# Kernel tuning notes

Measured on AMD Instinct MI355X. Metric: run time of the kernel, lower is better.

Reference implementation:

```python
import jax, jax.numpy as jnp
import numpy as np

B, S, DM, H, D = 2, 1024, 1024, 16, 64  # batch, seq, d_model, heads, head_dim


def setup_inputs() -> dict:
    key = jax.random.key(0)
    ks = jax.random.split(key, 16)
    sc = 1.0 / np.sqrt(DM)
    scd = 1.0 / np.sqrt(D)
    return {
        "hidden_states": jax.random.normal(ks[0], (B, S, DM), dtype=jnp.float32),
        # frozen base_attn projections
        "Wq": jax.random.normal(ks[1], (DM, DM), dtype=jnp.float32) * sc,
        "bq": jnp.zeros((DM,), dtype=jnp.float32),
        "Wk": jax.random.normal(ks[2], (DM, DM), dtype=jnp.float32) * sc,
        "bk": jnp.zeros((DM,), dtype=jnp.float32),
        "Wv": jax.random.normal(ks[3], (DM, DM), dtype=jnp.float32) * sc,
        "bv": jnp.zeros((DM,), dtype=jnp.float32),
        "Wo": jax.random.normal(ks[4], (DM, DM), dtype=jnp.float32) * sc,
        "bo": jnp.zeros((DM,), dtype=jnp.float32),
        # trainable hedgehog feature maps (per-head Linear(head_dim, head_dim))
        "Wfq": jax.random.normal(ks[5], (D, D), dtype=jnp.float32) * scd,
        "bfq": jnp.zeros((D,), dtype=jnp.float32),
        "Wfk": jax.random.normal(ks[6], (D, D), dtype=jnp.float32) * scd,
        "bfk": jnp.zeros((D,), dtype=jnp.float32),
    }


def _heads(x):
    # (B, S, DM) -> (B, H, S, D)
    return x.reshape(B, S, H, D).transpose(0, 2, 1, 3)


def _feature_map(x, W, b):
    # HedgehogFeatureMap: Linear then concat(exp(x), exp(-x)) along last dim
    y = jnp.einsum('bhsd,ed->bhse', x, W) + b
    return jnp.concatenate([jnp.exp(y), jnp.exp(-y)], axis=-1)  # (B,H,S,2D)


def reference(hidden_states, Wq, bq, Wk, bk, Wv, bv, Wo, bo, Wfq, bfq, Wfk, bfk):
    # base_attn: standard multi-head softmax attention with output_attentions=True
    q = _heads(hidden_states @ Wq.T + bq)
    k = _heads(hidden_states @ Wk.T + bk)
    v = _heads(hidden_states @ Wv.T + bv)
    scores = jnp.einsum('bhmd,bhnd->bhmn', q, k) / jnp.sqrt(jnp.float32(D))
    true_attns = jax.nn.softmax(scores, axis=-1)  # (B,H,S,S)
    ctx = jnp.einsum('bhmn,bhnd->bhmd', true_attns, v)
    outputs = ctx.transpose(0, 2, 1, 3).reshape(B, S, DM) @ Wo.T + bo

    # hedgehog path: feature maps on q/k then sum-normalized quadratic attention
    fq = _feature_map(q, Wfq, bfq)
    fk = _feature_map(k, Wfk, bfk)
    qk = jnp.einsum('bhmd,bhnd->bhmn', fq, fk)
    pred_attns = qk / jnp.sum(qk, axis=-1, keepdims=True)
    return (outputs, pred_attns, true_attns)
```

## Files before the change

### kernel.cpp

```cpp
#include <hip/hip_runtime.h>
#include <math.h>

constexpr int B_ = 2, S_ = 1024, DM_ = 1024, NH_ = 16, HD_ = 64;
constexpr long SD = (long)S_ * DM_;
constexpr long SS = (long)S_ * S_;

typedef _Float16 half8 __attribute__((ext_vector_type(8)));
typedef _Float16 half4 __attribute__((ext_vector_type(4)));
typedef float floatx4 __attribute__((ext_vector_type(4)));

__device__ __forceinline__ void gl_lds16(const void* g, void* l) {
    __builtin_amdgcn_global_load_lds(
        (const __attribute__((address_space(1))) void*)g,
        (__attribute__((address_space(3))) void*)l, 16, 0, 0);
}

__global__ __launch_bounds__(256) void cvt_all(
    const float* __restrict__ hs,  const float* __restrict__ Wq,
    const float* __restrict__ Wk,  const float* __restrict__ Wv,
    const float* __restrict__ Wo,  const float* __restrict__ Wfq,
    const float* __restrict__ Wfk,
    _Float16* __restrict__ hsH, _Float16* __restrict__ WqH,
    _Float16* __restrict__ WkH, _Float16* __restrict__ WvH,
    _Float16* __restrict__ WoH, _Float16* __restrict__ WfqH,
    _Float16* __restrict__ WfkH)
{
    long i = (long)blockIdx.x * 256 + threadIdx.x;
    const float* src; _Float16* dst; long off;
    if (i < 524288)       { src = hs;  dst = hsH;  off = i; }
    else if (i < 786432)  { src = Wq;  dst = WqH;  off = i - 524288; }
    else if (i < 1048576) { src = Wk;  dst = WkH;  off = i - 786432; }
    else if (i < 1310720) { src = Wv;  dst = WvH;  off = i - 1048576; }
    else if (i < 1572864) { src = Wo;  dst = WoH;  off = i - 1310720; }
    else if (i < 1573888) { src = Wfq; dst = WfqH; off = i - 1572864; }
    else                  { src = Wfk; dst = WfkH; off = i - 1573888; }
    float4 v = ((const float4*)src)[off];
    half4 h = { (_Float16)v.x, (_Float16)v.y, (_Float16)v.z, (_Float16)v.w };
    ((half4*)dst)[off] = h;
}

template <int BM, int BN, int WM, int WN>
__global__ __launch_bounds__(256) void mm_nt(
    const _Float16* __restrict__ Ap, const _Float16* __restrict__ Wp,
    const float* __restrict__ bias, const float* __restrict__ rowscale,
    float* __restrict__ Cf,
    _Float16* __restrict__ Ch, int K, int lda, int ldw, int ldc,
    long sAb, long sAh, long sWb, long sWh, long sCb, long sCh,
    float scale, int mode)
{
    constexpr int MI = WM / 16, NI = WN / 16;
    const int z = blockIdx.z, b = z / NH_, h = z % NH_;
    const int wave = threadIdx.x >> 6, lane = threadIdx.x & 63;
    const int m0 = blockIdx.y * BM, n0 = blockIdx.x * BN;
    const int wm = (wave >> 1) * WM, wn = (wave & 1) * WN;
    const int r16 = lane & 15, quad = lane >> 4;

    const _Float16* Az = Ap + (long)b * sAb + (long)h * sAh;
    const _Float16* Wz = Wp + (long)b * sWb + (long)h * sWh;

    __shared__ __align__(16) _Float16 As[2 * BM * 32];
    __shared__ __align__(16) _Float16 Bs[2 * BN * 32];

    floatx4 acc[MI][NI];
#pragma unroll
    for (int i = 0; i < MI; ++i)
#pragma unroll
        for (int j = 0; j < NI; ++j)
#pragma unroll
            for (int r = 0; r < 4; ++r) acc[i][j][r] = 0.f;

    for (int k0 = 0; k0 < K; k0 += 64) {
#pragma unroll
        for (int hf = 0; hf < 2; ++hf) {
#pragma unroll
            for (int c = wave * (BM / 64); c < (wave + 1) * (BM / 64); ++c) {
                const _Float16* g = Az + (long)(m0 + c * 16 + (lane >> 2)) * lda
                                    + k0 + hf * 32 + (lane & 3) * 8;
                gl_lds16(g, &As[hf * BM * 32 + c * 512]);
            }
#pragma unroll
            for (int c = wave * (BN / 64); c < (wave + 1) * (BN / 64); ++c) {
                const _Float16* g = Wz + (long)(n0 + c * 16 + (lane >> 2)) * ldw
                                    + k0 + hf * 32 + (lane & 3) * 8;
                gl_lds16(g, &Bs[hf * BN * 32 + c * 512]);
            }
        }
        __syncthreads();

#pragma unroll
        for (int hf = 0; hf < 2; ++hf) {
            half8 af[MI], bf8[NI];
#pragma unroll
            for (int i = 0; i < MI; ++i)
                af[i] = *(const half8*)&As[hf * BM * 32
                                           + (wm + i * 16 + r16) * 32 + quad * 8];
#pragma unroll
            for (int j = 0; j < NI; ++j)
                bf8[j] = *(const half8*)&Bs[hf * BN * 32
                                            + (wn + j * 16 + r16) * 32 + quad * 8];
#pragma unroll
            for (int i = 0; i < MI; ++i)
#pragma unroll
                for (int j = 0; j < NI; ++j)
                    acc[i][j] = __builtin_amdgcn_mfma_f32_16x16x32_f16(
                        af[i], bf8[j], acc[i][j], 0, 0, 0);
        }
        __syncthreads();
    }

    const long cb = (long)b * sCb + (long)h * sCh;
#pragma unroll
    for (int i = 0; i < MI; ++i) {
#pragma unroll
        for (int j = 0; j < NI; ++j) {
#pragma unroll
            for (int r = 0; r < 4; ++r) {
                int row = m0 + wm + i * 16 + quad * 4 + r;
                int col = n0 + wn + j * 16 + r16;
                float v = acc[i][j][r] * scale;
                if (bias) v += bias[col];
                if (rowscale) v *= rowscale[(long)z * 1024 + row];
                if (mode == 0) Cf[cb + (long)row * ldc + col] = v;
                else           Ch[cb + (long)row * ldc + col] = (_Float16)v;
            }
        }
    }
}

__global__ __launch_bounds__(256) void qkv_proj(
    const _Float16* __restrict__ hsH,
    const _Float16* __restrict__ W0, const _Float16* __restrict__ W1,
    const _Float16* __restrict__ W2,
    const float* __restrict__ b0, const float* __restrict__ b1,
    const float* __restrict__ b2,
    _Float16* __restrict__ QH, _Float16* __restrict__ KH,
    _Float16* __restrict__ VtH)
{
    const int z = blockIdx.z;
    const _Float16* W = (z == 0) ? W0 : (z == 1) ? W1 : W2;
    const float* bias = (z == 0) ? b0 : (z == 1) ? b1 : b2;

    const int wave = threadIdx.x >> 6, lane = threadIdx.x & 63;
    const int m0 = blockIdx.y * 128, n0 = blockIdx.x * 128;
    const int wm = (wave >> 1) * 64, wn = (wave & 1) * 64;
    const int r16 = lane & 15, quad = lane >> 4;

    __shared__ __align__(16) _Float16 As[2 * 128 * 32];
    __shared__ __align__(16) _Float16 Bs[2 * 128 * 32];

    floatx4 acc[4][4];
#pragma unroll
    for (int i = 0; i < 4; ++i)
#pragma unroll
        for (int j = 0; j < 4; ++j)
#pragma unroll
            for (int r = 0; r < 4; ++r) acc[i][j][r] = 0.f;

    for (int k0 = 0; k0 < 1024; k0 += 64) {
#pragma unroll
        for (int hf = 0; hf < 2; ++hf) {
#pragma unroll
            for (int c = wave * 2; c < wave * 2 + 2; ++c) {
                const _Float16* ga = hsH + (long)(m0 + c * 16 + (lane >> 2)) * 1024
                                     + k0 + hf * 32 + (lane & 3) * 8;
                gl_lds16(ga, &As[hf * 4096 + c * 512]);
                const _Float16* gb = W + (long)(n0 + c * 16 + (lane >> 2)) * 1024
                                     + k0 + hf * 32 + (lane & 3) * 8;
                gl_lds16(gb, &Bs[hf * 4096 + c * 512]);
            }
        }
        __syncthreads();

#pragma unroll
        for (int hf = 0; hf < 2; ++hf) {
            half8 af[4], bf8[4];
#pragma unroll
            for (int i = 0; i < 4; ++i)
                af[i] = *(const half8*)&As[hf * 4096
                                           + (wm + i * 16 + r16) * 32 + quad * 8];
#pragma unroll
            for (int j = 0; j < 4; ++j)
                bf8[j] = *(const half8*)&Bs[hf * 4096
                                            + (wn + j * 16 + r16) * 32 + quad * 8];
#pragma unroll
            for (int i = 0; i < 4; ++i)
#pragma unroll
                for (int j = 0; j < 4; ++j)
                    acc[i][j] = __builtin_amdgcn_mfma_f32_16x16x32_f16(
                        af[i], bf8[j], acc[i][j], 0, 0, 0);
        }
        __syncthreads();
    }

    _Float16* dst = (z == 0) ? QH : KH;
#pragma unroll
    for (int i = 0; i < 4; ++i) {
#pragma unroll
        for (int j = 0; j < 4; ++j) {
#pragma unroll
            for (int r = 0; r < 4; ++r) {
                int row = m0 + wm + i * 16 + quad * 4 + r;
                int col = n0 + wn + j * 16 + r16;
                float v = acc[i][j][r] + bias[col];
                if (z < 2) {
                    dst[(long)row * 1024 + col] = (_Float16)v;
                } else {
                    int bb = row >> 10, s = row & 1023;
                    int hh = col >> 6, d = col & 63;
                    VtH[((((long)bb * 16 + hh) * 64 + d) << 10) | s] = (_Float16)v;
                }
            }
        }
    }
}

__global__ __launch_bounds__(512) void attn_fused(
    const _Float16* __restrict__ Q, const _Float16* __restrict__ K,
    const _Float16* __restrict__ Vt, float* __restrict__ trueA,
    _Float16* __restrict__ ctx)
{
    const int z = blockIdx.y, b = z >> 4, h = z & 15;
    const int m0 = blockIdx.x * 32;
    const int wave = threadIdx.x >> 6, lane = threadIdx.x & 63;
    const int r16 = lane & 15, quad = lane >> 4;
    const int c0 = wave * 128;

    __shared__ __align__(16) _Float16 Ps[32 * 1024];
    float* redmx = (float*)Ps;
    float* redsm = (float*)Ps + 256;
    float* kred  = (float*)Ps;

    const _Float16* Qb = Q + (long)b * SD + h * 64;
    const _Float16* Kb = K + (long)b * SD + h * 64;

    half8 af[2][2];
#pragma unroll
    for (int mi = 0; mi < 2; ++mi)
#pragma unroll
        for (int ks = 0; ks < 2; ++ks)
            af[mi][ks] = *(const half8*)&Qb[(long)(m0 + mi * 16 + r16) * DM_
                                            + ks * 32 + quad * 8];

    floatx4 acc[2][8];
#pragma unroll
    for (int mi = 0; mi < 2; ++mi)
#pragma unroll
        for (int nj = 0; nj < 8; ++nj)
#pragma unroll
            for (int r = 0; r < 4; ++r) acc[mi][nj][r] = 0.f;

#pragma unroll
    for (int ks = 0; ks < 2; ++ks) {
#pragma unroll
        for (int nj = 0; nj < 8; ++nj) {
            half8 bf = *(const half8*)&Kb[(long)(c0 + nj * 16 + r16) * DM_
                                          + ks * 32 + quad * 8];
            acc[0][nj] = __builtin_amdgcn_mfma_f32_16x16x32_f16(
                af[0][ks], bf, acc[0][nj], 0, 0, 0);
            acc[1][nj] = __builtin_amdgcn_mfma_f32_16x16x32_f16(
                af[1][ks], bf, acc[1][nj], 0, 0, 0);
        }
    }

    float rmx[2][4];
#pragma unroll
    for (int mi = 0; mi < 2; ++mi)
#pragma unroll
        for (int r = 0; r < 4; ++r) {
            float m = acc[mi][0][r];
#pragma unroll
            for (int nj = 1; nj < 8; ++nj) m = fmaxf(m, acc[mi][nj][r]);
#pragma unroll
            for (int o = 1; o <= 8; o <<= 1) m = fmaxf(m, __shfl_xor(m, o, 64));
            rmx[mi][r] = m;
        }
    if (r16 == 0) {
#pragma unroll
        for (int mi = 0; mi < 2; ++mi)
#pragma unroll
            for (int r = 0; r < 4; ++r)
                redmx[wave * 32 + mi * 16 + quad * 4 + r] = rmx[mi][r];
    }
    __syncthreads();
    float mx[2][4];
#pragma unroll
    for (int mi = 0; mi < 2; ++mi)
#pragma unroll
        for (int r = 0; r < 4; ++r) {
            float m = redmx[mi * 16 + quad * 4 + r];
#pragma unroll
            for (int w = 1; w < 8; ++w)
                m = fmaxf(m, redmx[w * 32 + mi * 16 + quad * 4 + r]);
            mx[mi][r] = m;
        }

    float rsm[2][4];
#pragma unroll
    for (int mi = 0; mi < 2; ++mi)
#pragma unroll
        for (int r = 0; r < 4; ++r) {
            float s = 0.f;
#pragma unroll
            for (int nj = 0; nj < 8; ++nj) {
                float p = __expf((acc[mi][nj][r] - mx[mi][r]) * 0.125f);
                acc[mi][nj][r] = p;
                s += p;
            }
#pragma unroll
            for (int o = 1; o <= 8; o <<= 1) s += __shfl_xor(s, o, 64);
            rsm[mi][r] = s;
        }
    if (r16 == 0) {
#pragma unroll
        for (int mi = 0; mi < 2; ++mi)
#pragma unroll
            for (int r = 0; r < 4; ++r)
                redsm[wave * 32 + mi * 16 + quad * 4 + r] = rsm[mi][r];
    }
    __syncthreads();
    float inv[2][4];
#pragma unroll
    for (int mi = 0; mi < 2; ++mi)
#pragma unroll
        for (int r = 0; r < 4; ++r) {
            float s = 0.f;
#pragma unroll
            for (int w = 0; w < 8; ++w)
                s += redsm[w * 32 + mi * 16 + quad * 4 + r];
            inv[mi][r] = 1.f / s;
        }
    __syncthreads();

    float* Ta = trueA + (long)z * SS + (long)m0 * S_;
#pragma unroll
    for (int mi = 0; mi < 2; ++mi) {
#pragma unroll
        for (int r = 0; r < 4; ++r) {
            const int row = mi * 16 + quad * 4 + r;
            const int sw = (row & 7) << 3;
            const float iv = inv[mi][r];
#pragma unroll
            for (int nj = 0; nj < 8; ++nj) {
                const int col = c0 + nj * 16 + r16;
                const float v = acc[mi][nj][r] * iv;
                Ta[(long)row * S_ + col] = v;
                Ps[row * 1024 + (col ^ sw)] = (_Float16)v;
            }
        }
    }
    __syncthreads();

    const int d0 = (wave & 3) * 16, kr = wave >> 2;
    const _Float16* Vb = Vt + ((long)z * 64 + d0 + r16) * (long)S_;
    floatx4 c2[2];
#pragma unroll
    for (int mi = 0; mi < 2; ++mi)
#pragma unroll
        for (int r = 0; r < 4; ++r) c2[mi][r] = 0.f;

    const int swz = (r16 & 7) << 3;
#pragma unroll 4
    for (int k0 = kr * 512; k0 < kr * 512 + 512; k0 += 32) {
        half8 pa0 = *(const half8*)&Ps[r16 * 1024 + ((k0 + quad * 8) ^ swz)];
        half8 pa1 = *(const half8*)&Ps[(16 + r16) * 1024 + ((k0 + quad * 8) ^ swz)];
        half8 vf  = *(const half8*)&Vb[k0 + quad * 8];
        c2[0] = __builtin_amdgcn_mfma_f32_16x16x32_f16(pa0, vf, c2[0], 0, 0, 0);
        c2[1] = __builtin_amdgcn_mfma_f32_16x16x32_f16(pa1, vf, c2[1], 0, 0, 0);
    }

    __syncthreads();
    if (kr == 1) {
#pragma unroll
        for (int mi = 0; mi < 2; ++mi)
            *(floatx4*)&kred[(((wave & 3) * 2 + mi) * 64 + lane) * 4] = c2[mi];
    }
    __syncthreads();
    if (kr == 0) {
        _Float16* Cb = ctx + (long)b * SD + h * 64;
#pragma unroll
        for (int mi = 0; mi < 2; ++mi) {
            c2[mi] += *(const floatx4*)&kred[((wave * 2 + mi) * 64 + lane) * 4];
#pragma unroll
            for (int r = 0; r < 4; ++r) {
                const int srow = m0 + mi * 16 + quad * 4 + r;
                Cb[(long)srow * DM_ + d0 + r16] = (_Float16)c2[mi][r];
            }
        }
    }
}

__global__ __launch_bounds__(256) void feat_map2(
    const _Float16* __restrict__ QH, const _Float16* __restrict__ KH,
    const _Float16* __restrict__ Wfq, const _Float16* __restrict__ Wfk,
    const float* __restrict__ bfq, const float* __restrict__ bfk,
    _Float16* __restrict__ fqH, _Float16* __restrict__ fkH,
    float* __restrict__ skp)
{
    const int which = blockIdx.z;
    const _Float16* Xh = which ? KH : QH;
    const _Float16* Wf = which ? Wfk : Wfq;
    const float* bf    = which ? bfk : bfq;
    _Float16* outH     = which ? fkH : fqH;

    const int z = blockIdx.y, b = z >> 4, h = z & 15;
    const int mb = blockIdx.x, m0 = mb * 64;
    __shared__ float Xs[64][65];
    __shared__ float Ws[64][65];
    __shared__ float red[16][128];
    const _Float16* Xb = Xh + (long)b * SD + h * 64;
    for (int i = threadIdx.x; i < 4096; i += 256) {
        int r = i >> 6, c = i & 63;
        Xs[r][c] = (float)Xb[(long)(m0 + r) * 1024 + c];
        Ws[r][c] = (float)Wf[i];
    }
    __syncthreads();
    const int tmg = threadIdx.x >> 4;
    const int tm = tmg * 4, tn = (threadIdx.x & 15) * 4;
    float acc[4][4] = {{0.f}};
    for (int k = 0; k < 64; ++k) {
        float xv[4], wv[4];
#pragma unroll
        for (int i = 0; i < 4; ++i) xv[i] = Xs[tm + i][k];
#pragma unroll
        for (int j = 0; j < 4; ++j) wv[j] = Ws[tn + j][k];
#pragma unroll
        for (int i = 0; i < 4; ++i)
#pragma unroll
            for (int j = 0; j < 4; ++j) acc[i][j] = fmaf(xv[i], wv[j], acc[i][j]);
    }
    float sp[4] = {0.f, 0.f, 0.f, 0.f}, sn[4] = {0.f, 0.f, 0.f, 0.f};
#pragma unroll
    for (int i = 0; i < 4; ++i) {
        long base = ((long)z * S_ + m0 + tm + i) * 128;
#pragma unroll
        for (int j = 0; j < 4; ++j) {
            float y = acc[i][j] + bf[tn + j];
            float ep = expf(y), en = expf(-y);
            outH[base + tn + j]      = (_Float16)ep;
            outH[base + 64 + tn + j] = (_Float16)en;
            sp[j] += ep; sn[j] += en;
        }
    }
    if (which) {
#pragma unroll
        for (int j = 0; j < 4; ++j) {
            red[tmg][tn + j]      = sp[j];
            red[tmg][64 + tn + j] = sn[j];
        }
        __syncthreads();
        if (threadIdx.x < 128) {
            float s = 0.f;
#pragma unroll
            for (int g = 0; g < 16; ++g) s += red[g][threadIdx.x];
            skp[((long)z * 16 + mb) * 128 + threadIdx.x] = s;
        }
    }
}

__global__ __launch_bounds__(256) void rowsum_inv(
    const _Float16* __restrict__ fqH, const float* __restrict__ skp,
    float* __restrict__ rsinv)
{
    const int g = blockIdx.x * 256 + threadIdx.x;
    const int z = g >> 10;
    __shared__ float skz[128];
    if (threadIdx.x < 128) {
        float s = 0.f;
#pragma unroll
        for (int m = 0; m < 16; ++m)
            s += skp[((long)z * 16 + m) * 128 + threadIdx.x];
        skz[threadIdx.x] = s;
    }
    __syncthreads();
    const _Float16* p = fqH + (long)g * 128;
    float acc = 0.f;
#pragma unroll
    for (int d0 = 0; d0 < 128; d0 += 8) {
        half8 v = *(const half8*)(p + d0);
#pragma unroll
        for (int j = 0; j < 8; ++j) acc = fmaf((float)v[j], skz[d0 + j], acc);
    }
    rsinv[g] = 1.f / acc;
}

extern "C" void kernel_launch(void* const* d_in, const int* in_sizes, int n_in,
                              void* d_out, int out_size, void* d_ws, size_t ws_size,
                              hipStream_t stream)
{
    (void)in_sizes; (void)n_in; (void)out_size; (void)ws_size;

    const float* hs  = (const float*)d_in[0];
    const float* Wq  = (const float*)d_in[1];
    const float* bq  = (const float*)d_in[2];
    const float* Wk  = (const float*)d_in[3];
    const float* bk  = (const float*)d_in[4];
    const float* Wv  = (const float*)d_in[5];
    const float* bv  = (const float*)d_in[6];
    const float* Wo  = (const float*)d_in[7];
    const float* bo  = (const float*)d_in[8];
    const float* Wfq = (const float*)d_in[9];
    const float* bfq = (const float*)d_in[10];
    const float* Wfk = (const float*)d_in[11];
    const float* bfk = (const float*)d_in[12];

    float* out0  = (float*)d_out;
    float* pred  = out0 + (long)B_ * S_ * DM_;
    float* trueA = pred + (long)B_ * NH_ * S_ * S_;

    _Float16* hsH  = (_Float16*)d_ws;
    _Float16* WqH  = hsH + 2 * 1024 * 1024;
    _Float16* WkH  = WqH + 1024 * 1024;
    _Float16* WvH  = WkH + 1024 * 1024;
    _Float16* WoH  = WvH + 1024 * 1024;
    _Float16* WfqH = WoH + 1024 * 1024;
    _Float16* WfkH = WfqH + 4096;
    _Float16* QH   = WfkH + 4096;
    _Float16* KH   = QH + 2 * 1024 * 1024;
    _Float16* VtH  = KH + 2 * 1024 * 1024;
    _Float16* ctxH = VtH + 2 * 1024 * 1024;
    _Float16* fqH  = ctxH + 2 * 1024 * 1024;
    _Float16* fkH  = fqH + (long)B_ * NH_ * S_ * 128;

    float* skp   = (float*)WqH;
    float* rsinv = (float*)WkH;

    const dim3 blk(256);

    cvt_all<<<6152, blk, 0, stream>>>(
        hs, Wq, Wk, Wv, Wo, Wfq, Wfk,
        hsH, WqH, WkH, WvH, WoH, WfqH, WfkH);

    qkv_proj<<<dim3(8, 16, 3), blk, 0, stream>>>(
        hsH, WqH, WkH, WvH, bq, bk, bv, QH, KH, VtH);

    attn_fused<<<dim3(32, 32), dim3(512), 0, stream>>>(
        QH, KH, VtH, trueA, ctxH);

    mm_nt<64, 128, 32, 64><<<dim3(8, 32, 1), blk, 0, stream>>>(
        ctxH, WoH, bo, nullptr, out0, nullptr, 1024, 1024, 1024, 1024,
        0, 0, 0, 0, 0, 0, 1.f, 0);

    feat_map2<<<dim3(16, 32, 2), blk, 0, stream>>>(
        QH, KH, WfqH, WfkH, bfq, bfk, fqH, fkH, skp);

    rowsum_inv<<<128, blk, 0, stream>>>(fqH, skp, rsinv);

    mm_nt<128, 128, 64, 64><<<dim3(8, 8, 32), blk, 0, stream>>>(
        fqH, fkH, nullptr, rsinv, pred, nullptr, 128, 128, 128, 1024,
        (long)16 * S_ * 128, (long)S_ * 128,
        (long)16 * S_ * 128, (long)S_ * 128,
        16 * SS, SS, 1.f, 0);
}
```

Baseline: 456.5 us.

## Fuse rowsum into pred GEMM, nontemporal stores, retile projections and PV loop

Removes the separate rowsum_inv kernel by computing the per-row normalizer inside the prediction GEMM prologue from skp and fq rows. Output stores for the large attention matrices become nontemporal to avoid cache pollution. QKV projection and output projection use smaller tiles for more blocks, and the attention PV product drops the split-K LDS reduction in favour of one wave per 16x16 output tile. This trades redundant normalizer recomputation per block and more tiles for fewer launches and syncs.

New measurement: 457.3 us. No clear change (+0.2%).

```diff
diff --git a/kernel.cpp b/kernel.cpp
--- a/kernel.cpp
+++ b/kernel.cpp
@@ -42,7 +42,7 @@
 template <int BM, int BN, int WM, int WN>
 __global__ __launch_bounds__(256) void mm_nt(
     const _Float16* __restrict__ Ap, const _Float16* __restrict__ Wp,
-    const float* __restrict__ bias, const float* __restrict__ rowscale,
+    const float* __restrict__ bias, const float* __restrict__ skp,
     float* __restrict__ Cf,
     _Float16* __restrict__ Ch, int K, int lda, int ldw, int ldc,
     long sAb, long sAh, long sWb, long sWh, long sCb, long sCh,
@@ -60,6 +60,31 @@
 
     __shared__ __align__(16) _Float16 As[2 * BM * 32];
     __shared__ __align__(16) _Float16 Bs[2 * BN * 32];
+    __shared__ float skz[128];
+    __shared__ float rsinvs[BM];
+
+    if (skp) {
+        if (threadIdx.x < 128) {
+            float s = 0.f;
+#pragma unroll
+            for (int m = 0; m < 16; ++m)
+                s += skp[((long)z * 16 + m) * 128 + threadIdx.x];
+            skz[threadIdx.x] = s;
+        }
+        __syncthreads();
+        if (threadIdx.x < BM) {
+            const _Float16* p = Az + (long)(m0 + threadIdx.x) * lda;
+            float acc = 0.f;
+#pragma unroll
+            for (int d0 = 0; d0 < 128; d0 += 8) {
+                half8 v = *(const half8*)(p + d0);
+#pragma unroll
+                for (int j = 0; j < 8; ++j)
+                    acc = fmaf((float)v[j], skz[d0 + j], acc);
+            }
+            rsinvs[threadIdx.x] = 1.f / acc;
+        }
+    }
 
     floatx4 acc[MI][NI];
 #pragma unroll
@@ -119,9 +144,11 @@
                 int col = n0 + wn + j * 16 + r16;
                 float v = acc[i][j][r] * scale;
                 if (bias) v += bias[col];
-                if (rowscale) v *= rowscale[(long)z * 1024 + row];
-                if (mode == 0) Cf[cb + (long)row * ldc + col] = v;
-                else           Ch[cb + (long)row * ldc + col] = (_Float16)v;
+                if (skp) v *= rsinvs[row - m0];
+                if (mode == 0)
+                    __builtin_nontemporal_store(v, &Cf[cb + (long)row * ldc + col]);
+                else
+                    Ch[cb + (long)row * ldc + col] = (_Float16)v;
             }
         }
     }
@@ -141,16 +168,16 @@
     const float* bias = (z == 0) ? b0 : (z == 1) ? b1 : b2;
 
     const int wave = threadIdx.x >> 6, lane = threadIdx.x & 63;
-    const int m0 = blockIdx.y * 128, n0 = blockIdx.x * 128;
-    const int wm = (wave >> 1) * 64, wn = (wave & 1) * 64;
+    const int m0 = blockIdx.y * 64, n0 = blockIdx.x * 128;
+    const int wm = (wave >> 1) * 32, wn = (wave & 1) * 64;
     const int r16 = lane & 15, quad = lane >> 4;
 
-    __shared__ __align__(16) _Float16 As[2 * 128 * 32];
+    __shared__ __align__(16) _Float16 As[2 * 64 * 32];
     __shared__ __align__(16) _Float16 Bs[2 * 128 * 32];
 
-    floatx4 acc[4][4];
-#pragma unroll
-    for (int i = 0; i < 4; ++i)
+    floatx4 acc[2][4];
+#pragma unroll
+    for (int i = 0; i < 2; ++i)
 #pragma unroll
         for (int j = 0; j < 4; ++j)
 #pragma unroll
@@ -159,11 +186,11 @@
     for (int k0 = 0; k0 < 1024; k0 += 64) {
 #pragma unroll
         for (int hf = 0; hf < 2; ++hf) {
+            const _Float16* ga = hsH + (long)(m0 + wave * 16 + (lane >> 2)) * 1024
+                                 + k0 + hf * 32 + (lane & 3) * 8;
+            gl_lds16(ga, &As[hf * 2048 + wave * 512]);
 #pragma unroll
             for (int c = wave * 2; c < wave * 2 + 2; ++c) {
-                const _Float16* ga = hsH + (long)(m0 + c * 16 + (lane >> 2)) * 1024
-                                     + k0 + hf * 32 + (lane & 3) * 8;
-                gl_lds16(ga, &As[hf * 4096 + c * 512]);
                 const _Float16* gb = W + (long)(n0 + c * 16 + (lane >> 2)) * 1024
                                      + k0 + hf * 32 + (lane & 3) * 8;
                 gl_lds16(gb, &Bs[hf * 4096 + c * 512]);
@@ -173,17 +200,17 @@
 
 #pragma unroll
         for (int hf = 0; hf < 2; ++hf) {
-            half8 af[4], bf8[4];
-#pragma unroll
-            for (int i = 0; i < 4; ++i)
-                af[i] = *(const half8*)&As[hf * 4096
+            half8 af[2], bf8[4];
+#pragma unroll
+            for (int i = 0; i < 2; ++i)
+                af[i] = *(const half8*)&As[hf * 2048
                                            + (wm + i * 16 + r16) * 32 + quad * 8];
 #pragma unroll
             for (int j = 0; j < 4; ++j)
                 bf8[j] = *(const half8*)&Bs[hf * 4096
                                             + (wn + j * 16 + r16) * 32 + quad * 8];
 #pragma unroll
-            for (int i = 0; i < 4; ++i)
+            for (int i = 0; i < 2; ++i)
 #pragma unroll
                 for (int j = 0; j < 4; ++j)
                     acc[i][j] = __builtin_amdgcn_mfma_f32_16x16x32_f16(
@@ -194,7 +221,7 @@
 
     _Float16* dst = (z == 0) ? QH : KH;
 #pragma unroll
-    for (int i = 0; i < 4; ++i) {
+    for (int i = 0; i < 2; ++i) {
 #pragma unroll
         for (int j = 0; j < 4; ++j) {
 #pragma unroll
@@ -228,7 +255,6 @@
     __shared__ __align__(16) _Float16 Ps[32 * 1024];
     float* redmx = (float*)Ps;
     float* redsm = (float*)Ps + 256;
-    float* kred  = (float*)Ps;
 
     const _Float16* Qb = Q + (long)b * SD + h * 64;
     const _Float16* Kb = K + (long)b * SD + h * 64;
@@ -343,49 +369,33 @@
             for (int nj = 0; nj < 8; ++nj) {
                 const int col = c0 + nj * 16 + r16;
                 const float v = acc[mi][nj][r] * iv;
-                Ta[(long)row * S_ + col] = v;
+                __builtin_nontemporal_store(v, &Ta[(long)row * S_ + col]);
                 Ps[row * 1024 + (col ^ sw)] = (_Float16)v;
             }
         }
     }
     __syncthreads();
 
-    const int d0 = (wave & 3) * 16, kr = wave >> 2;
+    const int mi = wave >> 2, d0 = (wave & 3) * 16;
     const _Float16* Vb = Vt + ((long)z * 64 + d0 + r16) * (long)S_;
-    floatx4 c2[2];
-#pragma unroll
-    for (int mi = 0; mi < 2; ++mi)
-#pragma unroll
-        for (int r = 0; r < 4; ++r) c2[mi][r] = 0.f;
+    floatx4 c2;
+#pragma unroll
+    for (int r = 0; r < 4; ++r) c2[r] = 0.f;
 
     const int swz = (r16 & 7) << 3;
-#pragma unroll 4
-    for (int k0 = kr * 512; k0 < kr * 512 + 512; k0 += 32) {
-        half8 pa0 = *(const half8*)&Ps[r16 * 1024 + ((k0 + quad * 8) ^ swz)];
-        half8 pa1 = *(const half8*)&Ps[(16 + r16) * 1024 + ((k0 + quad * 8) ^ swz)];
-        half8 vf  = *(const half8*)&Vb[k0 + quad * 8];
-        c2[0] = __builtin_amdgcn_mfma_f32_16x16x32_f16(pa0, vf, c2[0], 0, 0, 0);
-        c2[1] = __builtin_amdgcn_mfma_f32_16x16x32_f16(pa1, vf, c2[1], 0, 0, 0);
-    }
-
-    __syncthreads();
-    if (kr == 1) {
-#pragma unroll
-        for (int mi = 0; mi < 2; ++mi)
-            *(floatx4*)&kred[(((wave & 3) * 2 + mi) * 64 + lane) * 4] = c2[mi];
-    }
-    __syncthreads();
-    if (kr == 0) {
-        _Float16* Cb = ctx + (long)b * SD + h * 64;
-#pragma unroll
-        for (int mi = 0; mi < 2; ++mi) {
-            c2[mi] += *(const floatx4*)&kred[((wave * 2 + mi) * 64 + lane) * 4];
-#pragma unroll
-            for (int r = 0; r < 4; ++r) {
-                const int srow = m0 + mi * 16 + quad * 4 + r;
-                Cb[(long)srow * DM_ + d0 + r16] = (_Float16)c2[mi][r];
-            }
-        }
+#pragma unroll 8
+    for (int k0 = 0; k0 < 1024; k0 += 32) {
+        half8 pa = *(const half8*)&Ps[(mi * 16 + r16) * 1024
+                                      + ((k0 + quad * 8) ^ swz)];
+        half8 vf = *(const half8*)&Vb[k0 + quad * 8];
+        c2 = __builtin_amdgcn_mfma_f32_16x16x32_f16(pa, vf, c2, 0, 0, 0);
+    }
+
+    _Float16* Cb = ctx + (long)b * SD + h * 64;
+#pragma unroll
+    for (int r = 0; r < 4; ++r) {
+        const int srow = m0 + mi * 16 + quad * 4 + r;
+        Cb[(long)srow * DM_ + d0 + r16] = (_Float16)c2[r];
     }
 }
 
@@ -455,32 +465,6 @@
             skp[((long)z * 16 + mb) * 128 + threadIdx.x] = s;
         }
     }
-}
-
-__global__ __launch_bounds__(256) void rowsum_inv(
-    const _Float16* __restrict__ fqH, const float* __restrict__ skp,
-    float* __restrict__ rsinv)
-{
-    const int g = blockIdx.x * 256 + threadIdx.x;
-    const int z = g >> 10;
-    __shared__ float skz[128];
-    if (threadIdx.x < 128) {
-        float s = 0.f;
-#pragma unroll
-        for (int m = 0; m < 16; ++m)
-            s += skp[((long)z * 16 + m) * 128 + threadIdx.x];
-        skz[threadIdx.x] = s;
-    }
-    __syncthreads();
-    const _Float16* p = fqH + (long)g * 128;
-    float acc = 0.f;
-#pragma unroll
-    for (int d0 = 0; d0 < 128; d0 += 8) {
-        half8 v = *(const half8*)(p + d0);
-#pragma unroll
-        for (int j = 0; j < 8; ++j) acc = fmaf((float)v[j], skz[d0 + j], acc);
-    }
-    rsinv[g] = 1.f / acc;
 }
 
 extern "C" void kernel_launch(void* const* d_in, const int* in_sizes, int n_in,
@@ -521,8 +505,7 @@
     _Float16* fqH  = ctxH + 2 * 1024 * 1024;
     _Float16* fkH  = fqH + (long)B_ * NH_ * S_ * 128;
 
-    float* skp   = (float*)WqH;
-    float* rsinv = (float*)WkH;
+    float* skp = (float*)WqH;
 
     const dim3 blk(256);
 
@@ -530,23 +513,21 @@
         hs, Wq, Wk, Wv, Wo, Wfq, Wfk,
         hsH, WqH, WkH, WvH, WoH, WfqH, WfkH);
 
-    qkv_proj<<<dim3(8, 16, 3), blk, 0, stream>>>(
+    qkv_proj<<<dim3(8, 32, 3), blk, 0, stream>>>(
         hsH, WqH, WkH, WvH, bq, bk, bv, QH, KH, VtH);
 
     attn_fused<<<dim3(32, 32), dim3(512), 0, stream>>>(
         QH, KH, VtH, trueA, ctxH);
 
-    mm_nt<64, 128, 32, 64><<<dim3(8, 32, 1), blk, 0, stream>>>(
+    mm_nt<64, 64, 32, 32><<<dim3(16, 32, 1), blk, 0, stream>>>(
         ctxH, WoH, bo, nullptr, out0, nullptr, 1024, 1024, 1024, 1024,
         0, 0, 0, 0, 0, 0, 1.f, 0);
 
     feat_map2<<<dim3(16, 32, 2), blk, 0, stream>>>(
         QH, KH, WfqH, WfkH, bfq, bfk, fqH, fkH, skp);
 
-    rowsum_inv<<<128, blk, 0, stream>>>(fqH, skp, rsinv);
-
     mm_nt<128, 128, 64, 64><<<dim3(8, 8, 32), blk, 0, stream>>>(
-        fqH, fkH, nullptr, rsinv, pred, nullptr, 128, 128, 128, 1024,
+        fqH, fkH, nullptr, skp, pred, nullptr, 128, 128, 128, 1024,
         (long)16 * S_ * 128, (long)S_ * 128,
         (long)16 * S_ * 128, (long)S_ * 128,
         16 * SS, SS, 1.f, 0);
```
